# Performance work log

Measured on AMD Instinct MI355X. Metric: run time of the kernel, lower is better.

The kernel has to match this reference:

```python
import jax, jax.numpy as jnp
import numpy as np

N = 35709   # vertices
F = 70789   # triangles
B = 64
CAMERA_DISTANCE = 10.0
FOCAL = 1015.0
IMAGE_SIZE = 224

SH_A = (np.pi, 2 * np.pi / np.sqrt(3.0), 2 * np.pi / np.sqrt(8.0))
SH_C = (1 / np.sqrt(4 * np.pi), np.sqrt(3.0) / np.sqrt(4 * np.pi), 3 * np.sqrt(5.0) / np.sqrt(12 * np.pi))


def _persc_proj():
    center = IMAGE_SIZE / 2
    m = np.array([FOCAL, 0, center, 0, FOCAL, center, 0, 0, 1], dtype=np.float32).reshape(3, 3).T
    return jnp.asarray(m)


def setup_inputs() -> dict:
    key = jax.random.key(0)
    ks = jax.random.split(key, 9)
    return {
        "coeffs": jax.random.normal(ks[0], (B, 257), jnp.float32),
        "meanshape": jax.random.normal(ks[1], (3 * N,), jnp.float32),
        "idBase": jax.random.normal(ks[2], (3 * N, 80), jnp.float32),
        "exBase": jax.random.normal(ks[3], (3 * N, 64), jnp.float32),
        "meantex": jax.random.uniform(ks[4], (3 * N,), jnp.float32) * 255.0,
        "texBase": jax.random.normal(ks[5], (3 * N, 80), jnp.float32),
        "persc_proj": _persc_proj(),
        "init_lit": jnp.array([0.8, 0, 0, 0, 0, 0, 0, 0, 0], jnp.float32).reshape(1, 1, 9),
        "point_buf": jax.random.randint(ks[6], (N, 8), 0, F + 1),   # index F = zero-pad row
        "face_buf": jax.random.randint(ks[7], (F, 3), 0, N),
        "keypoints": jax.random.randint(ks[8], (68,), 0, N),
    }


def _l2norm(x):
    # matches torch F.normalize(p=2, eps=1e-12)
    return x / jnp.maximum(jnp.linalg.norm(x, axis=-1, keepdims=True), 1e-12)


def _rotation(angles):
    x, y, z = angles[:, 0], angles[:, 1], angles[:, 2]
    o, zr = jnp.ones_like(x), jnp.zeros_like(x)
    cx, sx = jnp.cos(x), jnp.sin(x)
    cy, sy = jnp.cos(y), jnp.sin(y)
    cz, sz = jnp.cos(z), jnp.sin(z)
    rx = jnp.stack([o, zr, zr, zr, cx, -sx, zr, sx, cx], -1).reshape(-1, 3, 3)
    ry = jnp.stack([cy, zr, sy, zr, o, zr, -sy, zr, cy], -1).reshape(-1, 3, 3)
    rz = jnp.stack([cz, -sz, zr, sz, cz, zr, zr, zr, o], -1).reshape(-1, 3, 3)
    return jnp.transpose(rz @ ry @ rx, (0, 2, 1))


def _compute_norm(face_shape, face_buf, point_buf):
    tri = face_shape[:, face_buf]                 # (B, F, 3verts, 3xyz) gather
    e1 = tri[:, :, 0] - tri[:, :, 1]
    e2 = tri[:, :, 1] - tri[:, :, 2]
    fn = _l2norm(jnp.cross(e1, e2))               # (B, F, 3)
    fn = jnp.concatenate([fn, jnp.zeros((fn.shape[0], 1, 3), fn.dtype)], axis=1)
    vn = jnp.sum(fn[:, point_buf], axis=2)        # (B, N, 3) gather-sum over 8 faces
    return _l2norm(vn)


def _compute_color(face_texture, face_norm, gamma, init_lit):
    a, c = SH_A, SH_C
    g = gamma.reshape(gamma.shape[0], 3, 9) + init_lit   # (B, 3, 9)
    g = jnp.transpose(g, (0, 2, 1))                      # (B, 9, 3)
    nx, ny, nz = face_norm[..., 0:1], face_norm[..., 1:2], face_norm[..., 2:3]
    Y = jnp.concatenate([
        a[0] * c[0] * jnp.ones_like(nx),
        -a[1] * c[1] * ny,
        a[1] * c[1] * nz,
        -a[1] * c[1] * nx,
        a[2] * c[2] * nx * ny,
        -a[2] * c[2] * ny * nz,
        0.5 * a[2] * c[2] / np.sqrt(3.0) * (3 * nz ** 2 - 1),
        -a[2] * c[2] * nx * nz,
        0.5 * a[2] * c[2] * (nx ** 2 - ny ** 2)], axis=-1)   # (B, N, 9)
    rgb = jnp.einsum('bnk,bkc->bnc', Y, g)
    return rgb * face_texture


def reference(coeffs, meanshape, idBase, exBase, meantex, texBase, persc_proj, init_lit, point_buf, face_buf, keypoints):
    id_c, ex_c, tex_c = coeffs[:, 0:80], coeffs[:, 80:144], coeffs[:, 144:224]
    angles, gamma, trans = coeffs[:, 224:227], coeffs[:, 227:254], coeffs[:, 254:257]
    Bsz = coeffs.shape[0]
    # shape blending (dense GEMMs)
    shape_flat = (jnp.einsum('ij,aj->ai', idBase, id_c)
                  + jnp.einsum('ij,aj->ai', exBase, ex_c)
                  + meanshape[None])
    face_shape = shape_flat.reshape(Bsz, -1, 3)
    rot = _rotation(angles)
    face_shape_t = face_shape @ rot + trans[:, None, :]
    # to camera: z -> camera_distance - z
    face_vertex = jnp.concatenate([face_shape_t[..., :2], CAMERA_DISTANCE - face_shape_t[..., 2:]], axis=-1)
    # perspective projection
    proj = face_vertex @ persc_proj
    face_proj = proj[..., :2] / proj[..., 2:]
    landmark = face_proj[:, keypoints, :]
    # texture blending
    face_texture = ((jnp.einsum('ij,aj->ai', texBase, tex_c) + meantex[None]) / 255.0).reshape(Bsz, -1, 3)
    # mesh normals on untransformed shape, rotated into camera frame
    face_norm = _compute_norm(face_shape, face_buf, point_buf)
    face_norm_r = face_norm @ rot
    face_color = _compute_color(face_texture, face_norm_r, gamma, init_lit)
    return face_vertex, face_color, landmark
```

## Files before the change

### kernel.cpp

```cpp
#include <hip/hip_runtime.h>

#define N_V 35709
#define N_F 70789
#define NR  (3*N_V)
#define NB  64

#define WS_ROT    0
#define WS_GM     576
#define WS_CTRS   2304
#define WS_CTRT   11520
#define WS_SHAPET 16640

__global__ __launch_bounds__(64) void k_setup_rot(
    const float* __restrict__ coeffs, const float* __restrict__ init_lit,
    float* __restrict__ rotM, float* __restrict__ gm)
{
    int b = threadIdx.x;
    const float* cb = coeffs + b * 257;

    float ax = cb[224], ay = cb[225], az = cb[226];
    float cx = cosf(ax), sx = sinf(ax);
    float cy = cosf(ay), sy = sinf(ay);
    float cz = cosf(az), sz = sinf(az);
    float m[9];
    m[0] = cz * cy;
    m[1] = cz * sy * sx - sz * cx;
    m[2] = sz * sx + cz * sy * cx;
    m[3] = sz * cy;
    m[4] = cz * cx + sz * sy * sx;
    m[5] = sz * sy * cx - cz * sx;
    m[6] = -sy;
    m[7] = cy * sx;
    m[8] = cy * cx;
#pragma unroll
    for (int k = 0; k < 9; k++) rotM[b * 9 + k] = m[k];

#pragma unroll
    for (int k = 0; k < 9; k++) {
        float il = init_lit[k];
#pragma unroll
        for (int c = 0; c < 3; c++)
            gm[b * 27 + k * 3 + c] = cb[227 + c * 9 + k] + il;
    }
}

__global__ __launch_bounds__(64) void k_transpose(
    const float* __restrict__ coeffs,
    float* __restrict__ ctrS, float* __restrict__ ctrT)
{
    int j = blockIdx.x;
    int b = threadIdx.x;
    float v = coeffs[b * 257 + j];
    if (j < 144) ctrS[j * 64 + b] = v;
    else         ctrT[(j - 144) * 64 + b] = v;
}

__global__ __launch_bounds__(256) void k_gemm(
    const float* __restrict__ idBase, const float* __restrict__ exBase,
    const float* __restrict__ texBase, const float* __restrict__ meanshape,
    const float* __restrict__ meantex,
    const float* __restrict__ ctrS, const float* __restrict__ ctrT,
    float* __restrict__ shapeT,
    float* __restrict__ texT,
    int tex_transposed)
{
    __shared__ float tsh[4][64 * 33];
    int w    = threadIdx.x >> 6;
    int lane = threadIdx.x & 63;
    int h    = blockIdx.y;
    int i0w  = blockIdx.x * 256 + w * 64;
    int i    = i0w + lane;
    int iv   = (i < NR) ? i : (NR - 1);
    float* sh = tsh[w];

    float acc[32];

#pragma unroll
    for (int c = 0; c < 32; c++) acc[c] = 0.f;
    {
        const float4* r4 = (const float4*)(idBase + (size_t)iv * 80);
#pragma unroll 2
        for (int jq = 0; jq < 20; jq++) {
            float4 a4 = r4[jq];
            float as[4] = {a4.x, a4.y, a4.z, a4.w};
#pragma unroll
            for (int s = 0; s < 4; s++) {
                float a = as[s];
                const float4* cp = (const float4*)(ctrS + (jq * 4 + s) * 64 + h * 32);
#pragma unroll
                for (int q = 0; q < 8; q++) {
                    float4 c = cp[q];
                    acc[4 * q + 0] += a * c.x;
                    acc[4 * q + 1] += a * c.y;
                    acc[4 * q + 2] += a * c.z;
                    acc[4 * q + 3] += a * c.w;
                }
            }
        }
        const float4* e4 = (const float4*)(exBase + (size_t)iv * 64);
#pragma unroll 2
        for (int jq = 0; jq < 16; jq++) {
            float4 a4 = e4[jq];
            float as[4] = {a4.x, a4.y, a4.z, a4.w};
#pragma unroll
            for (int s = 0; s < 4; s++) {
                float a = as[s];
                const float4* cp = (const float4*)(ctrS + (80 + jq * 4 + s) * 64 + h * 32);
#pragma unroll
                for (int q = 0; q < 8; q++) {
                    float4 c = cp[q];
                    acc[4 * q + 0] += a * c.x;
                    acc[4 * q + 1] += a * c.y;
                    acc[4 * q + 2] += a * c.z;
                    acc[4 * q + 3] += a * c.w;
                }
            }
        }
        float ms = meanshape[iv];
#pragma unroll
        for (int c = 0; c < 32; c++) sh[lane * 33 + c] = acc[c] + ms;
#pragma unroll 4
        for (int it = 0; it < 32; it++) {
            int r  = it * 2 + (lane >> 5);
            int cb = lane & 31;
            int rg = i0w + r;
            float v = sh[r * 33 + cb];
            if (rg < NR) shapeT[(size_t)rg * 64 + h * 32 + cb] = v;
        }
    }

#pragma unroll
    for (int c = 0; c < 32; c++) acc[c] = 0.f;
    {
        const float4* t4 = (const float4*)(texBase + (size_t)iv * 80);
#pragma unroll 2
        for (int jq = 0; jq < 20; jq++) {
            float4 a4 = t4[jq];
            float as[4] = {a4.x, a4.y, a4.z, a4.w};
#pragma unroll
            for (int s = 0; s < 4; s++) {
                float a = as[s];
                const float4* cp = (const float4*)(ctrT + (jq * 4 + s) * 64 + h * 32);
#pragma unroll
                for (int q = 0; q < 8; q++) {
                    float4 c = cp[q];
                    acc[4 * q + 0] += a * c.x;
                    acc[4 * q + 1] += a * c.y;
                    acc[4 * q + 2] += a * c.z;
                    acc[4 * q + 3] += a * c.w;
                }
            }
        }
        float mt = meantex[iv];
        const float inv255 = 1.0f / 255.0f;
        if (tex_transposed) {
#pragma unroll
            for (int c = 0; c < 32; c++) sh[lane * 33 + c] = (acc[c] + mt) * inv255;
#pragma unroll 4
            for (int it = 0; it < 32; it++) {
                int r  = it * 2 + (lane >> 5);
                int cb = lane & 31;
                int rg = i0w + r;
                float v = sh[r * 33 + cb];
                if (rg < NR) texT[(size_t)rg * 64 + h * 32 + cb] = v;
            }
        } else {
            if (i < NR) {
#pragma unroll
                for (int c = 0; c < 32; c++)
                    texT[(size_t)(h * 32 + c) * NR + i] = (acc[c] + mt) * inv255;
            }
        }
    }
}

__global__ __launch_bounds__(256) void k_facenorm(
    const float* __restrict__ shapeT,
    const int* __restrict__ face_buf,
    float* __restrict__ fnT)
{
    int wave = threadIdx.x >> 6;
    int b    = threadIdx.x & 63;
    int f0   = blockIdx.x * 32 + wave * 8;

#pragma unroll
    for (int fr = 0; fr < 8; fr++) {
        int f = f0 + fr;
        if (f < N_F) {
            int i0 = face_buf[f * 3 + 0];
            int i1 = face_buf[f * 3 + 1];
            int i2 = face_buf[f * 3 + 2];
            float p0x = shapeT[(size_t)(3 * i0)     * 64 + b];
            float p0y = shapeT[(size_t)(3 * i0 + 1) * 64 + b];
            float p0z = shapeT[(size_t)(3 * i0 + 2) * 64 + b];
            float p1x = shapeT[(size_t)(3 * i1)     * 64 + b];
            float p1y = shapeT[(size_t)(3 * i1 + 1) * 64 + b];
            float p1z = shapeT[(size_t)(3 * i1 + 2) * 64 + b];
            float p2x = shapeT[(size_t)(3 * i2)     * 64 + b];
            float p2y = shapeT[(size_t)(3 * i2 + 1) * 64 + b];
            float p2z = shapeT[(size_t)(3 * i2 + 2) * 64 + b];
            float e1x = p0x - p1x, e1y = p0y - p1y, e1z = p0z - p1z;
            float e2x = p1x - p2x, e2y = p1y - p2y, e2z = p1z - p2z;
            float ccx = e1y * e2z - e1z * e2y;
            float ccy = e1z * e2x - e1x * e2z;
            float ccz = e1x * e2y - e1y * e2x;
            float l = sqrtf(ccx * ccx + ccy * ccy + ccz * ccz);
            float inv = 1.0f / fmaxf(l, 1e-12f);
            fnT[(size_t)(3 * f)     * 64 + b] = ccx * inv;
            fnT[(size_t)(3 * f + 1) * 64 + b] = ccy * inv;
            fnT[(size_t)(3 * f + 2) * 64 + b] = ccz * inv;
        }
    }
}

__global__ __launch_bounds__(256) void k_vertex_fn(
    const float* __restrict__ shapeT,
    const float* __restrict__ texT,
    const float* __restrict__ fnT,
    const float* __restrict__ rotM, const float* __restrict__ gm,
    const float* __restrict__ coeffs,
    const int* __restrict__ point_buf,
    float* __restrict__ out_vertex, float* __restrict__ out_color)
{
    __shared__ float sh[64 * 49];
    int wave = threadIdx.x >> 6;
    int b    = threadIdx.x & 63;
    int v0   = blockIdx.x * 16;
    int nvalid = N_V - v0; if (nvalid > 16) nvalid = 16;
    int kmax = 3 * nvalid;

    float m0 = rotM[b * 9 + 0], m1 = rotM[b * 9 + 1], m2 = rotM[b * 9 + 2];
    float m3 = rotM[b * 9 + 3], m4 = rotM[b * 9 + 4], m5 = rotM[b * 9 + 5];
    float m6 = rotM[b * 9 + 6], m7 = rotM[b * 9 + 7], m8 = rotM[b * 9 + 8];
    float tx = coeffs[b * 257 + 254], ty = coeffs[b * 257 + 255], tz = coeffs[b * 257 + 256];
    float g[27];
#pragma unroll
    for (int k = 0; k < 27; k++) g[k] = gm[b * 27 + k];

    const float A0C0 = 0.8862269254527580f;
    const float A1C1 = 1.7724538509055159f;
    const float A2C2 = 2.4270323912f;
    const float C6   = 0.7006239022f;
    const float C8   = 1.2135161956f;

    float vert[4][3];
    float col[4][3];

#pragma unroll
    for (int vr = 0; vr < 4; vr++) {
        int v = v0 + wave * 4 + vr;
        int vc = (v < N_V) ? v : (N_V - 1);

        float sx0 = shapeT[(size_t)(3 * vc)     * 64 + b];
        float sy0 = shapeT[(size_t)(3 * vc + 1) * 64 + b];
        float sz0 = shapeT[(size_t)(3 * vc + 2) * 64 + b];

        float vx = m0 * sx0 + m1 * sy0 + m2 * sz0 + tx;
        float vy = m3 * sx0 + m4 * sy0 + m5 * sz0 + ty;
        float vz = m6 * sx0 + m7 * sy0 + m8 * sz0 + tz;
        vert[vr][0] = vx; vert[vr][1] = vy; vert[vr][2] = 10.0f - vz;

        float nx = 0.f, ny = 0.f, nz = 0.f;
#pragma unroll
        for (int k = 0; k < 8; k++) {
            int f = point_buf[vc * 8 + k];
            if (f < N_F) {
                nx += fnT[(size_t)(3 * f)     * 64 + b];
                ny += fnT[(size_t)(3 * f + 1) * 64 + b];
                nz += fnT[(size_t)(3 * f + 2) * 64 + b];
            }
        }
        float l = sqrtf(nx * nx + ny * ny + nz * nz);
        float inv = 1.0f / fmaxf(l, 1e-12f);
        nx *= inv; ny *= inv; nz *= inv;

        float rx = m0 * nx + m1 * ny + m2 * nz;
        float ry = m3 * nx + m4 * ny + m5 * nz;
        float rz = m6 * nx + m7 * ny + m8 * nz;

        float Y0 = A0C0;
        float Y1 = -A1C1 * ry;
        float Y2 =  A1C1 * rz;
        float Y3 = -A1C1 * rx;
        float Y4 =  A2C2 * rx * ry;
        float Y5 = -A2C2 * ry * rz;
        float Y6 =  C6 * (3.f * rz * rz - 1.f);
        float Y7 = -A2C2 * rx * rz;
        float Y8 =  C8 * (rx * rx - ry * ry);

        float t0 = texT[(size_t)(3 * vc)     * 64 + b];
        float t1 = texT[(size_t)(3 * vc + 1) * 64 + b];
        float t2 = texT[(size_t)(3 * vc + 2) * 64 + b];
        float tex3[3] = {t0, t1, t2};
#pragma unroll
        for (int c = 0; c < 3; c++) {
            float rgb = Y0 * g[0 + c] + Y1 * g[3 + c] + Y2 * g[6 + c] + Y3 * g[9 + c] +
                        Y4 * g[12 + c] + Y5 * g[15 + c] + Y6 * g[18 + c] + Y7 * g[21 + c] +
                        Y8 * g[24 + c];
            col[vr][c] = rgb * tex3[c];
        }
    }

#pragma unroll
    for (int vr = 0; vr < 4; vr++)
#pragma unroll
        for (int c = 0; c < 3; c++)
            sh[b * 49 + (wave * 4 + vr) * 3 + c] = vert[vr][c];
    __syncthreads();
#pragma unroll 4
    for (int it = 0; it < 12; it++) {
        int f = it * 256 + threadIdx.x;
        int bb = f / 48, k = f - bb * 48;
        if (k < kmax)
            __builtin_nontemporal_store(sh[bb * 49 + k],
                                        out_vertex + (size_t)bb * NR + 3 * (size_t)v0 + k);
    }
    __syncthreads();

#pragma unroll
    for (int vr = 0; vr < 4; vr++)
#pragma unroll
        for (int c = 0; c < 3; c++)
            sh[b * 49 + (wave * 4 + vr) * 3 + c] = col[vr][c];
    __syncthreads();
#pragma unroll 4
    for (int it = 0; it < 12; it++) {
        int f = it * 256 + threadIdx.x;
        int bb = f / 48, k = f - bb * 48;
        if (k < kmax)
            __builtin_nontemporal_store(sh[bb * 49 + k],
                                        out_color + (size_t)bb * NR + 3 * (size_t)v0 + k);
    }
}

__global__ __launch_bounds__(256) void k_vertex(
    const float* __restrict__ shapeT,
    const float* __restrict__ texT,
    const float* __restrict__ rotM, const float* __restrict__ gm,
    const float* __restrict__ coeffs,
    const int* __restrict__ point_buf, const int* __restrict__ face_buf,
    float* __restrict__ out_vertex, float* __restrict__ out_color,
    int tex_in_out)
{
    __shared__ float sh[64 * 97];
    int wave = threadIdx.x >> 6;
    int b    = threadIdx.x & 63;
    int v0   = blockIdx.x * 32;
    int nvalid = N_V - v0; if (nvalid > 32) nvalid = 32;
    int kmax = 3 * nvalid;

    float m0 = rotM[b * 9 + 0], m1 = rotM[b * 9 + 1], m2 = rotM[b * 9 + 2];
    float m3 = rotM[b * 9 + 3], m4 = rotM[b * 9 + 4], m5 = rotM[b * 9 + 5];
    float m6 = rotM[b * 9 + 6], m7 = rotM[b * 9 + 7], m8 = rotM[b * 9 + 8];
    float tx = coeffs[b * 257 + 254], ty = coeffs[b * 257 + 255], tz = coeffs[b * 257 + 256];
    float g[27];
#pragma unroll
    for (int k = 0; k < 27; k++) g[k] = gm[b * 27 + k];

    const float A0C0 = 0.8862269254527580f;
    const float A1C1 = 1.7724538509055159f;
    const float A2C2 = 2.4270323912f;
    const float C6   = 0.7006239022f;
    const float C8   = 1.2135161956f;

    float vert[8][3];
    float col[8][3];

#pragma unroll
    for (int vr = 0; vr < 8; vr++) {
        int v = v0 + wave * 8 + vr;
        bool valid = (v < N_V);
        int vc = valid ? v : (N_V - 1);

        float sx0 = shapeT[(size_t)(3 * vc)     * 64 + b];
        float sy0 = shapeT[(size_t)(3 * vc + 1) * 64 + b];
        float sz0 = shapeT[(size_t)(3 * vc + 2) * 64 + b];

        float vx = m0 * sx0 + m1 * sy0 + m2 * sz0 + tx;
        float vy = m3 * sx0 + m4 * sy0 + m5 * sz0 + ty;
        float vz = m6 * sx0 + m7 * sy0 + m8 * sz0 + tz;
        vert[vr][0] = vx; vert[vr][1] = vy; vert[vr][2] = 10.0f - vz;

        float nx = 0.f, ny = 0.f, nz = 0.f;
#pragma unroll
        for (int k = 0; k < 8; k++) {
            int f = point_buf[vc * 8 + k];
            if (f < N_F) {
                int i0 = face_buf[f * 3], i1 = face_buf[f * 3 + 1], i2 = face_buf[f * 3 + 2];
                float p0x = shapeT[(size_t)(3 * i0)     * 64 + b];
                float p0y = shapeT[(size_t)(3 * i0 + 1) * 64 + b];
                float p0z = shapeT[(size_t)(3 * i0 + 2) * 64 + b];
                float p1x = shapeT[(size_t)(3 * i1)     * 64 + b];
                float p1y = shapeT[(size_t)(3 * i1 + 1) * 64 + b];
                float p1z = shapeT[(size_t)(3 * i1 + 2) * 64 + b];
                float p2x = shapeT[(size_t)(3 * i2)     * 64 + b];
                float p2y = shapeT[(size_t)(3 * i2 + 1) * 64 + b];
                float p2z = shapeT[(size_t)(3 * i2 + 2) * 64 + b];
                float e1x = p0x - p1x, e1y = p0y - p1y, e1z = p0z - p1z;
                float e2x = p1x - p2x, e2y = p1y - p2y, e2z = p1z - p2z;
                float ccx = e1y * e2z - e1z * e2y;
                float ccy = e1z * e2x - e1x * e2z;
                float ccz = e1x * e2y - e1y * e2x;
                float l = sqrtf(ccx * ccx + ccy * ccy + ccz * ccz);
                float inv = 1.0f / fmaxf(l, 1e-12f);
                nx += ccx * inv; ny += ccy * inv; nz += ccz * inv;
            }
        }
        float l = sqrtf(nx * nx + ny * ny + nz * nz);
        float inv = 1.0f / fmaxf(l, 1e-12f);
        nx *= inv; ny *= inv; nz *= inv;

        float rx = m0 * nx + m1 * ny + m2 * nz;
        float ry = m3 * nx + m4 * ny + m5 * nz;
        float rz = m6 * nx + m7 * ny + m8 * nz;

        float Y0 = A0C0;
        float Y1 = -A1C1 * ry;
        float Y2 =  A1C1 * rz;
        float Y3 = -A1C1 * rx;
        float Y4 =  A2C2 * rx * ry;
        float Y5 = -A2C2 * ry * rz;
        float Y6 =  C6 * (3.f * rz * rz - 1.f);
        float Y7 = -A2C2 * rx * rz;
        float Y8 =  C8 * (rx * rx - ry * ry);

        float t0, t1, t2;
        if (tex_in_out) {
            size_t ob = (size_t)b * NR + 3 * (size_t)vc;
            t0 = out_color[ob]; t1 = out_color[ob + 1]; t2 = out_color[ob + 2];
        } else {
            t0 = texT[(size_t)(3 * vc)     * 64 + b];
            t1 = texT[(size_t)(3 * vc + 1) * 64 + b];
            t2 = texT[(size_t)(3 * vc + 2) * 64 + b];
        }
        float tex3[3] = {t0, t1, t2};
#pragma unroll
        for (int c = 0; c < 3; c++) {
            float rgb = Y0 * g[0 + c] + Y1 * g[3 + c] + Y2 * g[6 + c] + Y3 * g[9 + c] +
                        Y4 * g[12 + c] + Y5 * g[15 + c] + Y6 * g[18 + c] + Y7 * g[21 + c] +
                        Y8 * g[24 + c];
            col[vr][c] = rgb * tex3[c];
        }
    }

#pragma unroll
    for (int vr = 0; vr < 8; vr++)
#pragma unroll
        for (int c = 0; c < 3; c++)
            sh[b * 97 + (wave * 8 + vr) * 3 + c] = vert[vr][c];
    __syncthreads();
#pragma unroll 4
    for (int it = 0; it < 24; it++) {
        int f = it * 256 + threadIdx.x;
        int bb = f / 96, k = f - bb * 96;
        if (k < kmax)
            __builtin_nontemporal_store(sh[bb * 97 + k],
                                        out_vertex + (size_t)bb * NR + 3 * (size_t)v0 + k);
    }
    __syncthreads();

#pragma unroll
    for (int vr = 0; vr < 8; vr++)
#pragma unroll
        for (int c = 0; c < 3; c++)
            sh[b * 97 + (wave * 8 + vr) * 3 + c] = col[vr][c];
    __syncthreads();
#pragma unroll 4
    for (int it = 0; it < 24; it++) {
        int f = it * 256 + threadIdx.x;
        int bb = f / 96, k = f - bb * 96;
        if (k < kmax)
            __builtin_nontemporal_store(sh[bb * 97 + k],
                                        out_color + (size_t)bb * NR + 3 * (size_t)v0 + k);
    }
}

__global__ __launch_bounds__(64) void k_landmark(
    const float* __restrict__ shapeT, const int* __restrict__ keypoints,
    const float* __restrict__ rotM, const float* __restrict__ coeffs,
    const float* __restrict__ P,
    float* __restrict__ out_lm)
{
    int l = blockIdx.x;
    int b = threadIdx.x;
    int kp = keypoints[l];

    float m0 = rotM[b * 9 + 0], m1 = rotM[b * 9 + 1], m2 = rotM[b * 9 + 2];
    float m3 = rotM[b * 9 + 3], m4 = rotM[b * 9 + 4], m5 = rotM[b * 9 + 5];
    float m6 = rotM[b * 9 + 6], m7 = rotM[b * 9 + 7], m8 = rotM[b * 9 + 8];
    float tx = coeffs[b * 257 + 254], ty = coeffs[b * 257 + 255], tz = coeffs[b * 257 + 256];

    float sx0 = shapeT[(size_t)(3 * kp)     * 64 + b];
    float sy0 = shapeT[(size_t)(3 * kp + 1) * 64 + b];
    float sz0 = shapeT[(size_t)(3 * kp + 2) * 64 + b];

    float x = m0 * sx0 + m1 * sy0 + m2 * sz0 + tx;
    float y = m3 * sx0 + m4 * sy0 + m5 * sz0 + ty;
    float z = 10.0f - (m6 * sx0 + m7 * sy0 + m8 * sz0 + tz);

    float p0 = x * P[0] + y * P[3] + z * P[6];
    float p1 = x * P[1] + y * P[4] + z * P[7];
    float p2 = x * P[2] + y * P[5] + z * P[8];

    size_t o = ((size_t)b * 68 + l) * 2;
    out_lm[o]     = p0 / p2;
    out_lm[o + 1] = p1 / p2;
}

extern "C" void kernel_launch(void* const* d_in, const int* in_sizes, int n_in,
                              void* d_out, int out_size, void* d_ws, size_t ws_size,
                              hipStream_t stream) {
    const float* coeffs    = (const float*)d_in[0];
    const float* meanshape = (const float*)d_in[1];
    const float* idBase    = (const float*)d_in[2];
    const float* exBase    = (const float*)d_in[3];
    const float* meantex   = (const float*)d_in[4];
    const float* texBase   = (const float*)d_in[5];
    const float* persc     = (const float*)d_in[6];
    const float* init_lit  = (const float*)d_in[7];
    const int*   point_buf = (const int*)d_in[8];
    const int*   face_buf  = (const int*)d_in[9];
    const int*   keypoints = (const int*)d_in[10];

    float* ws = (float*)d_ws;
    float* rotM   = ws + WS_ROT;
    float* gm     = ws + WS_GM;
    float* ctrS   = ws + WS_CTRS;
    float* ctrT   = ws + WS_CTRT;
    float* shapeT = ws + WS_SHAPET;

    float* out_vertex = (float*)d_out;
    float* out_color  = out_vertex + (size_t)NB * NR;
    float* out_lm     = out_color  + (size_t)NB * NR;

    size_t NRx64 = (size_t)NR * 64;
    size_t need_tex = ((size_t)WS_SHAPET + 2 * NRx64) * sizeof(float);
    size_t need_fn  = need_tex + (size_t)3 * N_F * 64 * sizeof(float);
    int tex_transposed = (ws_size >= need_tex) ? 1 : 0;
    int use_fn         = (ws_size >= need_fn) ? 1 : 0;
    float* texT = tex_transposed ? (shapeT + NRx64) : out_color;
    float* fnT  = shapeT + 2 * NRx64;

    k_setup_rot<<<1, 64, 0, stream>>>(coeffs, init_lit, rotM, gm);
    k_transpose<<<224, 64, 0, stream>>>(coeffs, ctrS, ctrT);

    dim3 gg((NR + 255) / 256, 2);
    k_gemm<<<gg, 256, 0, stream>>>(idBase, exBase, texBase, meanshape,
                                   meantex, ctrS, ctrT, shapeT, texT,
                                   tex_transposed);

    if (use_fn) {
        int fb = (N_F + 31) / 32;
        k_facenorm<<<fb, 256, 0, stream>>>(shapeT, face_buf, fnT);
        int vb = (N_V + 15) / 16;
        k_vertex_fn<<<vb, 256, 0, stream>>>(shapeT, texT, fnT, rotM, gm, coeffs,
                                            point_buf, out_vertex, out_color);
    } else {
        int vb = (N_V + 31) / 32;
        k_vertex<<<vb, 256, 0, stream>>>(shapeT, tex_transposed ? texT : nullptr,
                                         rotM, gm, coeffs, point_buf, face_buf,
                                         out_vertex, out_color,
                                         tex_transposed ? 0 : 1);
    }

    k_landmark<<<68, 64, 0, stream>>>(shapeT, keypoints, rotM, coeffs, persc, out_lm);
}
```

Measured before the change: 316.4 us.

## Interleave xyz per batch for face normals and hoist vertex gathers

Face normals are now stored interleaved as (face, batch, xyz), so one random gather brings in all three components from a single contiguous 12-byte chunk. A zero row at index N_F lets the vertex kernel drop its bounds branch. An optional repack kernel builds an xyz-interleaved copy of the shape for the face-normal gather. In the vertex kernel, point_buf indices, shape and texture loads are issued up front so more memory requests are in flight at once. The extra repack pass and higher register pressure may offset part of the gather savings.

```diff
diff --git a/kernel.cpp b/kernel.cpp
--- a/kernel.cpp
+++ b/kernel.cpp
@@ -174,15 +174,70 @@
     }
 }
 
+__global__ __launch_bounds__(256) void k_repack3(
+    const float* __restrict__ shapeT, float* __restrict__ shape3)
+{
+    int wave = threadIdx.x >> 6;
+    int b    = threadIdx.x & 63;
+    int v0   = blockIdx.x * 32 + wave * 8;
+#pragma unroll
+    for (int r = 0; r < 8; r++) {
+        int v = v0 + r;
+        if (v < N_V) {
+            float x = shapeT[(size_t)(3 * v)     * 64 + b];
+            float y = shapeT[(size_t)(3 * v + 1) * 64 + b];
+            float z = shapeT[(size_t)(3 * v + 2) * 64 + b];
+            float* o = shape3 + ((size_t)v * 64 + b) * 3;
+            o[0] = x; o[1] = y; o[2] = z;
+        }
+    }
+}
+
+__global__ __launch_bounds__(256) void k_facenorm3(
+    const float* __restrict__ shape3,
+    const int* __restrict__ face_buf,
+    float* __restrict__ fnT3)
+{
+    int wave = threadIdx.x >> 6;
+    int b    = threadIdx.x & 63;
+    int f0   = blockIdx.x * 32 + wave * 8;
+#pragma unroll
+    for (int fr = 0; fr < 8; fr++) {
+        int f = f0 + fr;
+        if (f < N_F) {
+            int i0 = face_buf[f * 3 + 0];
+            int i1 = face_buf[f * 3 + 1];
+            int i2 = face_buf[f * 3 + 2];
+            const float* p0 = shape3 + ((size_t)i0 * 64 + b) * 3;
+            const float* p1 = shape3 + ((size_t)i1 * 64 + b) * 3;
+            const float* p2 = shape3 + ((size_t)i2 * 64 + b) * 3;
+            float p0x = p0[0], p0y = p0[1], p0z = p0[2];
+            float p1x = p1[0], p1y = p1[1], p1z = p1[2];
+            float p2x = p2[0], p2y = p2[1], p2z = p2[2];
+            float e1x = p0x - p1x, e1y = p0y - p1y, e1z = p0z - p1z;
+            float e2x = p1x - p2x, e2y = p1y - p2y, e2z = p1z - p2z;
+            float ccx = e1y * e2z - e1z * e2y;
+            float ccy = e1z * e2x - e1x * e2z;
+            float ccz = e1x * e2y - e1y * e2x;
+            float l = sqrtf(ccx * ccx + ccy * ccy + ccz * ccz);
+            float inv = 1.0f / fmaxf(l, 1e-12f);
+            float* o = fnT3 + ((size_t)f * 64 + b) * 3;
+            o[0] = ccx * inv; o[1] = ccy * inv; o[2] = ccz * inv;
+        } else if (f == N_F) {
+            float* o = fnT3 + ((size_t)f * 64 + b) * 3;
+            o[0] = 0.f; o[1] = 0.f; o[2] = 0.f;
+        }
+    }
+}
+
 __global__ __launch_bounds__(256) void k_facenorm(
     const float* __restrict__ shapeT,
     const int* __restrict__ face_buf,
-    float* __restrict__ fnT)
+    float* __restrict__ fnT3)
 {
     int wave = threadIdx.x >> 6;
     int b    = threadIdx.x & 63;
     int f0   = blockIdx.x * 32 + wave * 8;
-
 #pragma unroll
     for (int fr = 0; fr < 8; fr++) {
         int f = f0 + fr;
@@ -206,9 +261,11 @@
             float ccz = e1x * e2y - e1y * e2x;
             float l = sqrtf(ccx * ccx + ccy * ccy + ccz * ccz);
             float inv = 1.0f / fmaxf(l, 1e-12f);
-            fnT[(size_t)(3 * f)     * 64 + b] = ccx * inv;
-            fnT[(size_t)(3 * f + 1) * 64 + b] = ccy * inv;
-            fnT[(size_t)(3 * f + 2) * 64 + b] = ccz * inv;
+            float* o = fnT3 + ((size_t)f * 64 + b) * 3;
+            o[0] = ccx * inv; o[1] = ccy * inv; o[2] = ccz * inv;
+        } else if (f == N_F) {
+            float* o = fnT3 + ((size_t)f * 64 + b) * 3;
+            o[0] = 0.f; o[1] = 0.f; o[2] = 0.f;
         }
     }
 }
@@ -216,7 +273,7 @@
 __global__ __launch_bounds__(256) void k_vertex_fn(
     const float* __restrict__ shapeT,
     const float* __restrict__ texT,
-    const float* __restrict__ fnT,
+    const float* __restrict__ fnT3,
     const float* __restrict__ rotM, const float* __restrict__ gm,
     const float* __restrict__ coeffs,
     const int* __restrict__ point_buf,
@@ -243,33 +300,43 @@
     const float C6   = 0.7006239022f;
     const float C8   = 1.2135161956f;
 
-    float vert[4][3];
-    float col[4][3];
-
+    int pf[4][8];
+    float sxv[4], syv[4], szv[4];
+    float t0v[4], t1v[4], t2v[4];
 #pragma unroll
     for (int vr = 0; vr < 4; vr++) {
         int v = v0 + wave * 4 + vr;
         int vc = (v < N_V) ? v : (N_V - 1);
-
-        float sx0 = shapeT[(size_t)(3 * vc)     * 64 + b];
-        float sy0 = shapeT[(size_t)(3 * vc + 1) * 64 + b];
-        float sz0 = shapeT[(size_t)(3 * vc + 2) * 64 + b];
-
-        float vx = m0 * sx0 + m1 * sy0 + m2 * sz0 + tx;
-        float vy = m3 * sx0 + m4 * sy0 + m5 * sz0 + ty;
-        float vz = m6 * sx0 + m7 * sy0 + m8 * sz0 + tz;
+#pragma unroll
+        for (int k = 0; k < 8; k++) pf[vr][k] = point_buf[vc * 8 + k];
+        sxv[vr] = shapeT[(size_t)(3 * vc)     * 64 + b];
+        syv[vr] = shapeT[(size_t)(3 * vc + 1) * 64 + b];
+        szv[vr] = shapeT[(size_t)(3 * vc + 2) * 64 + b];
+        t0v[vr] = texT[(size_t)(3 * vc)     * 64 + b];
+        t1v[vr] = texT[(size_t)(3 * vc + 1) * 64 + b];
+        t2v[vr] = texT[(size_t)(3 * vc + 2) * 64 + b];
+    }
+
+    float vert[4][3];
+    float col[4][3];
+
+#pragma unroll
+    for (int vr = 0; vr < 4; vr++) {
+        float fx[8], fy[8], fz[8];
+#pragma unroll
+        for (int k = 0; k < 8; k++) {
+            const float* fp = fnT3 + ((size_t)pf[vr][k] * 64 + b) * 3;
+            fx[k] = fp[0]; fy[k] = fp[1]; fz[k] = fp[2];
+        }
+
+        float vx = m0 * sxv[vr] + m1 * syv[vr] + m2 * szv[vr] + tx;
+        float vy = m3 * sxv[vr] + m4 * syv[vr] + m5 * szv[vr] + ty;
+        float vz = m6 * sxv[vr] + m7 * syv[vr] + m8 * szv[vr] + tz;
         vert[vr][0] = vx; vert[vr][1] = vy; vert[vr][2] = 10.0f - vz;
 
         float nx = 0.f, ny = 0.f, nz = 0.f;
 #pragma unroll
-        for (int k = 0; k < 8; k++) {
-            int f = point_buf[vc * 8 + k];
-            if (f < N_F) {
-                nx += fnT[(size_t)(3 * f)     * 64 + b];
-                ny += fnT[(size_t)(3 * f + 1) * 64 + b];
-                nz += fnT[(size_t)(3 * f + 2) * 64 + b];
-            }
-        }
+        for (int k = 0; k < 8; k++) { nx += fx[k]; ny += fy[k]; nz += fz[k]; }
         float l = sqrtf(nx * nx + ny * ny + nz * nz);
         float inv = 1.0f / fmaxf(l, 1e-12f);
         nx *= inv; ny *= inv; nz *= inv;
@@ -288,10 +355,7 @@
         float Y7 = -A2C2 * rx * rz;
         float Y8 =  C8 * (rx * rx - ry * ry);
 
-        float t0 = texT[(size_t)(3 * vc)     * 64 + b];
-        float t1 = texT[(size_t)(3 * vc + 1) * 64 + b];
-        float t2 = texT[(size_t)(3 * vc + 2) * 64 + b];
-        float tex3[3] = {t0, t1, t2};
+        float tex3[3] = {t0v[vr], t1v[vr], t2v[vr]};
 #pragma unroll
         for (int c = 0; c < 3; c++) {
             float rgb = Y0 * g[0 + c] + Y1 * g[3 + c] + Y2 * g[6 + c] + Y3 * g[9 + c] +
@@ -533,13 +597,21 @@
     float* out_color  = out_vertex + (size_t)NB * NR;
     float* out_lm     = out_color  + (size_t)NB * NR;
 
-    size_t NRx64 = (size_t)NR * 64;
+    size_t NRx64   = (size_t)NR * 64;
+    size_t fn3_len = (size_t)(N_F + 1) * 64 * 3;
+    size_t sh3_len = (size_t)N_V * 64 * 3;
+
     size_t need_tex = ((size_t)WS_SHAPET + 2 * NRx64) * sizeof(float);
-    size_t need_fn  = need_tex + (size_t)3 * N_F * 64 * sizeof(float);
+    size_t need_fn  = need_tex + fn3_len * sizeof(float);
+    size_t need_s3  = need_fn + sh3_len * sizeof(float);
+
     int tex_transposed = (ws_size >= need_tex) ? 1 : 0;
     int use_fn         = (ws_size >= need_fn) ? 1 : 0;
-    float* texT = tex_transposed ? (shapeT + NRx64) : out_color;
-    float* fnT  = shapeT + 2 * NRx64;
+    int use_s3         = (ws_size >= need_s3) ? 1 : 0;
+
+    float* texT   = tex_transposed ? (shapeT + NRx64) : out_color;
+    float* fnT3   = shapeT + 2 * NRx64;
+    float* shape3 = fnT3 + fn3_len;
 
     k_setup_rot<<<1, 64, 0, stream>>>(coeffs, init_lit, rotM, gm);
     k_transpose<<<224, 64, 0, stream>>>(coeffs, ctrS, ctrT);
@@ -550,10 +622,16 @@
                                    tex_transposed);
 
     if (use_fn) {
-        int fb = (N_F + 31) / 32;
-        k_facenorm<<<fb, 256, 0, stream>>>(shapeT, face_buf, fnT);
+        int fb = (N_F + 1 + 31) / 32;
+        if (use_s3) {
+            int rb = (N_V + 31) / 32;
+            k_repack3<<<rb, 256, 0, stream>>>(shapeT, shape3);
+            k_facenorm3<<<fb, 256, 0, stream>>>(shape3, face_buf, fnT3);
+        } else {
+            k_facenorm<<<fb, 256, 0, stream>>>(shapeT, face_buf, fnT3);
+        }
         int vb = (N_V + 15) / 16;
-        k_vertex_fn<<<vb, 256, 0, stream>>>(shapeT, texT, fnT, rotM, gm, coeffs,
+        k_vertex_fn<<<vb, 256, 0, stream>>>(shapeT, texT, fnT3, rotM, gm, coeffs,
                                             point_buf, out_vertex, out_color);
     } else {
         int vb = (N_V + 31) / 32;
```

Result: faster. 296.3 us (-6.4%).
